# Optimization experiments

Hardware: AMD Instinct MI355X
Metric: run time of the kernel (lower is better)

## Reference

```python
import jax, jax.numpy as jnp
import numpy as np

C = 256
C8 = C // 8
B, H, W = 4, 64, 64


def setup_inputs() -> dict:
    key = jax.random.key(0)
    ks = jax.random.split(key, 10)
    s = lambda fan_in: 1.0 / np.sqrt(fan_in)
    return {
        "x": jax.random.normal(ks[0], (B, C, H, W), dtype=jnp.float32),
        "conv_w": jax.random.normal(ks[1], (C8, C), dtype=jnp.float32) * s(C),
        "conv_b": jax.random.normal(ks[2], (C8,), dtype=jnp.float32) * 0.01,
        "q_w": jax.random.normal(ks[3], (C8, C8), dtype=jnp.float32) * s(C8),
        "q_b": jax.random.normal(ks[4], (C8,), dtype=jnp.float32) * 0.01,
        "k_w": jax.random.normal(ks[5], (C8, C8), dtype=jnp.float32) * s(C8),
        "k_b": jax.random.normal(ks[6], (C8,), dtype=jnp.float32) * 0.01,
        "v_w": jax.random.normal(ks[7], (C, C8), dtype=jnp.float32) * s(C8),
        "v_b": jax.random.normal(ks[8], (C,), dtype=jnp.float32) * 0.01,
        "gamma": jax.random.normal(ks[9], (1,), dtype=jnp.float32) * 0.1,
    }


def reference(x, conv_w, conv_b, q_w, q_b, k_w, k_b, v_w, v_b, gamma):
    b, c, h, w = x.shape
    hw = h * w
    # 1x1 convs are channel-mixing matmuls over flattened spatial dims
    xf = x.reshape(b, c, hw)                                   # [B, C, HW]
    proj = jnp.einsum('dc,bcn->bdn', conv_w, xf) + conv_b[None, :, None]   # [B, C8, HW]
    q = jnp.einsum('ed,bdn->bne', q_w, proj) + q_b[None, None, :]          # [B, HW, C8]
    k = jnp.einsum('ed,bdn->ben', k_w, proj) + k_b[None, :, None]          # [B, C8, HW]
    v = jnp.einsum('cd,bdn->bcn', v_w, proj) + v_b[None, :, None]          # [B, C, HW]
    attn = jax.nn.softmax(jnp.einsum('bne,bem->bnm', q, k), axis=-1)       # [B, HW, HW]
    out = jnp.einsum('bcm,bnm->bcn', v, attn)                              # [B, C, HW]
    out = out.reshape(b, c, h, w)
    return gamma[0] * out + x
```

## Files before the change

kernel.cpp:

```cpp
#include <hip/hip_runtime.h>
#include <hip/hip_bf16.h>
#include <stdint.h>

#define B_   4
#define C_   256
#define C8_  32
#define HW_  4096
#define ROWS_ 320
#define MS_  4
#define L2E  1.4426950408889634f

typedef __attribute__((ext_vector_type(8)))  short  short8;
typedef __attribute__((ext_vector_type(8)))  ushort us8;
typedef __attribute__((ext_vector_type(16))) float  f32x16;

#define WT_OFF    0
#define BALL_OFF  (256*320*4)
#define Q_OFF     (BALL_OFF + 1280)
#define KT_OFF    (Q_OFF  + B_*HW_*C8_*2)
#define V_OFF     (KT_OFF + B_*HW_*C8_*2)
#define PACC_OFF  (V_OFF  + B_*C_*HW_*2)
#define LPART_OFF (PACC_OFF + (size_t)MS_*B_*C_*HW_*2)

__device__ __forceinline__ ushort f2bf(float f) {
    union { float f; uint32_t u; } v; v.f = f;
    uint32_t u = v.u;
    uint32_t r = u + 0x7fffu + ((u >> 16) & 1u);
    return (ushort)(r >> 16);
}
__device__ __forceinline__ uint32_t pktr(float lo, float hi) {
    union { float f; uint32_t u; } a, b; a.f = lo; b.f = hi;
    return __builtin_amdgcn_perm(b.u, a.u, 0x07060302u);
}
__device__ __forceinline__ float fexp2(float s) {
    float y = fmaf(s, 8388608.0f, 1064992506.0f);
    y = fmaxf(y, 0.0f);
    union { int i; float f; } c; c.i = (int)y;
    return c.f;
}

__global__ __launch_bounds__(256) void k_setup(
    const float* __restrict__ conv_w, const float* __restrict__ conv_b,
    const float* __restrict__ q_w, const float* __restrict__ q_b,
    const float* __restrict__ k_w, const float* __restrict__ k_b,
    const float* __restrict__ v_w, const float* __restrict__ v_b,
    ushort* __restrict__ wbf, float* __restrict__ ball)
{
    int r = blockIdx.x;
    int c = threadIdx.x;
    const float* wrow;
    float bias;
    if (r < 32)       { wrow = q_w + r*32;      bias = q_b[r];      }
    else if (r < 64)  { wrow = k_w + (r-32)*32; bias = k_b[r-32];   }
    else              { wrow = v_w + (r-64)*32; bias = v_b[r-64];   }
    float acc = 0.f;
    #pragma unroll
    for (int d = 0; d < 32; ++d) acc += wrow[d] * conv_w[d*C_ + c];
    float scale = (r < 32) ? L2E : 1.0f;
    int lanew = (r & 31) + 32*((c >> 3) & 1);
    int fidx  = (c >> 4)*10 + (r >> 5);
    wbf[fidx*512 + lanew*8 + (c & 7)] = f2bf(acc * scale);
    if (c == 0) {
        float bb = bias;
        #pragma unroll
        for (int d = 0; d < 32; ++d) bb += wrow[d] * conv_b[d];
        ball[r] = bb * scale;
    }
}

__global__ __launch_bounds__(320) void k_qkv(
    const float* __restrict__ x, const ushort* __restrict__ wbf,
    const float* __restrict__ ball,
    ushort* __restrict__ qg, ushort* __restrict__ ktg, ushort* __restrict__ vg)
{
    __shared__ ushort tr[5][32*40];

    int blk = blockIdx.x;
    int b  = blk >> 7;
    int nt = blk & 127;
    int n0 = nt * 32;
    int t = threadIdx.x;
    int w = t >> 6, lane = t & 63;
    int l31 = lane & 31, h = lane >> 5;

    f32x16 acc[2];
    acc[0] = (f32x16)(0.f);
    acc[1] = (f32x16)(0.f);

    const float* xb = x + (size_t)b*C_*HW_ + n0 + l31;

    #pragma unroll 2
    for (int kc = 0; kc < 16; ++kc) {
        short8 a0 = *(const short8*)(wbf + (kc*10 + w*2    )*512 + lane*8);
        short8 a1 = *(const short8*)(wbf + (kc*10 + w*2 + 1)*512 + lane*8);
        const float* xc = xb + (size_t)(kc*16 + h*8)*HW_;
        union { uint32_t d[4]; short8 s8; } bf;
        #pragma unroll
        for (int j2 = 0; j2 < 4; ++j2) {
            float f0 = xc[(size_t)(2*j2    )*HW_];
            float f1 = xc[(size_t)(2*j2 + 1)*HW_];
            bf.d[j2] = pktr(f0, f1);
        }
        acc[0] = __builtin_amdgcn_mfma_f32_32x32x16_bf16(a0, bf.s8, acc[0], 0, 0, 0);
        acc[1] = __builtin_amdgcn_mfma_f32_32x32x16_bf16(a1, bf.s8, acc[1], 0, 0, 0);
    }

    #pragma unroll
    for (int mi = 0; mi < 2; ++mi) {
        int rowb = w*64 + mi*32;
        bool isQK = (rowb < 64);
        #pragma unroll
        for (int r = 0; r < 16; ++r) {
            int roff = (r & 3) + 8*(r >> 2) + 4*h;
            ushort bv = f2bf(acc[mi][r] + ball[rowb + roff]);
            int ad = isQK ? (l31*40 + roff) : (roff*40 + l31);
            tr[w][ad] = bv;
        }
        __syncthreads();
        #pragma unroll
        for (int f = 0; f < 2; ++f) {
            us8 frag = *(const us8*)(&tr[w][l31*40 + f*16 + h*8]);
            if (isQK) {
                ushort* dstb = (rowb == 0) ? qg : ktg;
                size_t ad = ((size_t)((b*128 + nt)*2 + f) << 9) + lane*8;
                *(us8*)(dstb + ad) = frag;
            } else {
                int cblk = (rowb - 64) >> 5;
                int mb = nt*2 + f;
                size_t ad = ((size_t)((b*8 + cblk)*256 + mb) << 9) + lane*8;
                *(us8*)(vg + ad) = frag;
            }
        }
        __syncthreads();
    }
}

__global__ __launch_bounds__(512, 4) void k_attn(
    const ushort* __restrict__ qg, const ushort* __restrict__ ktg,
    const ushort* __restrict__ vg,
    ushort* __restrict__ pacc, float* __restrict__ lpart)
{
    __shared__ ushort v_lds[2][16*512];
    __shared__ ushort kt_lds[2][4*512];

    int blk = blockIdx.x;
    int ms = blk & 3;
    int cs = (blk >> 2) & 1;
    int qb = (blk >> 3) & 15;
    int b  = blk >> 7;
    int t = threadIdx.x;
    int w = t >> 6, lane = t & 63;
    int l31 = lane & 31, h = lane >> 5;
    int mbase = ms*1024;

    short8 qf[2];
    #pragma unroll
    for (int ks = 0; ks < 2; ++ks)
        qf[ks] = *(const short8*)(qg
            + ((size_t)((b*128 + qb*8 + w)*2 + ks) << 9) + lane*8);

    f32x16 acc[4];
    #pragma unroll
    for (int j = 0; j < 4; ++j) acc[j] = (f32x16)(0.f);
    float lsum = 0.f;

    #define STAGE(buf, m0)                                                          \
    {                                                                               \
        _Pragma("unroll")                                                           \
        for (int ff = 0; ff < 2; ++ff) {                                            \
            int f = w*2 + ff;                                                       \
            int cfr = f >> 2, mf = f & 3;                                           \
            const ushort* src = vg + ((size_t)((b*8 + cs*4 + cfr)*256               \
                                 + ((m0) >> 4) + mf) << 9) + lane*8;                \
            __builtin_amdgcn_global_load_lds(                                       \
                (const __attribute__((address_space(1))) uint32_t*)src,             \
                (__attribute__((address_space(3))) uint32_t*)&v_lds[buf][f*512],    \
                16, 0, 0);                                                          \
        }                                                                           \
        if (w < 4) {                                                                \
            const ushort* src = ktg + ((size_t)((b*128 + ((m0) >> 5) + (w >> 1))*2  \
                                 + (w & 1)) << 9) + lane*8;                         \
            __builtin_amdgcn_global_load_lds(                                       \
                (const __attribute__((address_space(1))) uint32_t*)src,             \
                (__attribute__((address_space(3))) uint32_t*)&kt_lds[buf][w*512],   \
                16, 0, 0);                                                          \
        }                                                                           \
    }

    STAGE(0, mbase)
    __syncthreads();

    int buf = 0;
    for (int it = 0; it < 16; ++it) {
        if (it + 1 < 16) STAGE(buf ^ 1, mbase + (it+1)*64)

        #pragma unroll
        for (int kb = 0; kb < 2; ++kb) {
            short8 kt0 = *(const short8*)(&kt_lds[buf][(kb*2+0)*512 + lane*8]);
            short8 kt1 = *(const short8*)(&kt_lds[buf][(kb*2+1)*512 + lane*8]);

            f32x16 s = (f32x16)(0.f);
            s = __builtin_amdgcn_mfma_f32_32x32x16_bf16(kt0, qf[0], s, 0, 0, 0);
            s = __builtin_amdgcn_mfma_f32_32x32x16_bf16(kt1, qf[1], s, 0, 0, 0);
            float e[16];
            #pragma unroll
            for (int r = 0; r < 16; ++r) e[r] = fexp2(s[r]);
            float t0 = 0.f, t1 = 0.f;
            #pragma unroll
            for (int r = 0; r < 8; ++r) { t0 += e[2*r]; t1 += e[2*r+1]; }
            lsum += t0 + t1;
            uint32_t u[8];
            #pragma unroll
            for (int i = 0; i < 8; ++i) u[i] = pktr(e[2*i], e[2*i+1]);

            uint32_t bpA = (uint32_t)__shfl_xor((int)(h ? u[0] : u[2]), 32);
            uint32_t bpB = (uint32_t)__shfl_xor((int)(h ? u[1] : u[3]), 32);
            uint32_t bpC = (uint32_t)__shfl_xor((int)(h ? u[4] : u[6]), 32);
            uint32_t bpD = (uint32_t)__shfl_xor((int)(h ? u[5] : u[7]), 32);
            union { uint32_t d[4]; short8 s8; } fe, fo;
            fe.d[0] = h ? bpA : u[0];  fe.d[1] = h ? bpB : u[1];
            fe.d[2] = h ? u[2] : bpA;  fe.d[3] = h ? u[3] : bpB;
            fo.d[0] = h ? bpC : u[4];  fo.d[1] = h ? bpD : u[5];
            fo.d[2] = h ? u[6] : bpC;  fo.d[3] = h ? u[7] : bpD;
            short8 pf0 = fe.s8;
            short8 pf1 = fo.s8;

            #pragma unroll
            for (int msub = 0; msub < 2; ++msub) {
                int ks16 = kb*2 + msub;
                short8 pfm = msub ? pf1 : pf0;
                #pragma unroll
                for (int cfr = 0; cfr < 4; ++cfr) {
                    short8 vf = *(const short8*)(&v_lds[buf][(cfr*4 + ks16)*512 + lane*8]);
                    acc[cfr] = __builtin_amdgcn_mfma_f32_32x32x16_bf16(vf, pfm, acc[cfr], 0, 0, 0);
                }
            }
        }
        __syncthreads();
        buf ^= 1;
    }

    {
        union { float f; int i; } cv; cv.f = lsum;
        cv.i = __shfl_xor(cv.i, 32);
        lsum += cv.f;
    }
    if (cs == 0 && h == 0)
        lpart[(size_t)(ms*B_ + b)*HW_ + qb*256 + w*32 + l31] = lsum;

    int blkl = ((ms*B_ + b)*16 + qb)*2 + cs;
    #pragma unroll
    for (int cfr = 0; cfr < 4; ++cfr) {
        union { uint32_t d[8]; us8 hlf[2]; } pk;
        #pragma unroll
        for (int i = 0; i < 8; ++i)
            pk.d[i] = pktr(acc[cfr][2*i], acc[cfr][2*i+1]);
        ushort* dst = pacc + ((size_t)(blkl*32 + w*4 + cfr) << 10);
        *(us8*)(dst + lane*8)       = pk.hlf[0];
        *(us8*)(dst + 512 + lane*8) = pk.hlf[1];
    }
    #undef STAGE
}

__global__ __launch_bounds__(256) void k_comb(
    const ushort* __restrict__ pacc, const float* __restrict__ lpart,
    const float* __restrict__ x, const float* __restrict__ gamma_p,
    float* __restrict__ out)
{
    int gid = blockIdx.x * 256 + threadIdx.x;
    int l31 = gid & 31;
    int h   = (gid >> 5) & 1;
    int cfr = (gid >> 6) & 3;
    int w   = (gid >> 8) & 7;
    int cs  = (gid >> 11) & 1;
    int qb  = (gid >> 12) & 15;
    int b   = (gid >> 16) & 3;

    int q = qb*256 + w*32 + l31;
    int frag = w*4 + cfr;
    int lane = h*32 + l31;

    float sum[16];
    #pragma unroll
    for (int k = 0; k < 16; ++k) sum[k] = 0.f;
    float lt = 0.f;

    #pragma unroll
    for (int ms = 0; ms < MS_; ++ms) {
        int blkl = ((ms*B_ + b)*16 + qb)*2 + cs;
        const ushort* pp = pacc + ((size_t)(blkl*32 + frag) << 10) + lane*8;
        us8 a0 = *(const us8*)pp;
        us8 a1 = *(const us8*)(pp + 512);
        #pragma unroll
        for (int k = 0; k < 8; ++k) {
            union { uint32_t u; float f; } cv;
            cv.u = ((uint32_t)a0[k]) << 16;  sum[k]   += cv.f;
            cv.u = ((uint32_t)a1[k]) << 16;  sum[k+8] += cv.f;
        }
        lt += lpart[(size_t)(ms*B_ + b)*HW_ + q];
    }

    float g = gamma_p[0];
    float rl = g / lt;
    const float* xb = x + (size_t)b*C_*HW_ + q;
    float* ob = out + (size_t)b*C_*HW_ + q;
    #pragma unroll
    for (int k = 0; k < 16; ++k) {
        int c = cs*128 + cfr*32 + (k & 3) + 8*(k >> 2) + 4*h;
        size_t idx = (size_t)c*HW_;
        ob[idx] = sum[k]*rl + xb[idx];
    }
}

extern "C" void kernel_launch(void* const* d_in, const int* in_sizes, int n_in,
                              void* d_out, int out_size, void* d_ws, size_t ws_size,
                              hipStream_t stream)
{
    const float* x      = (const float*)d_in[0];
    const float* conv_w = (const float*)d_in[1];
    const float* conv_b = (const float*)d_in[2];
    const float* q_w    = (const float*)d_in[3];
    const float* q_b    = (const float*)d_in[4];
    const float* k_w    = (const float*)d_in[5];
    const float* k_b    = (const float*)d_in[6];
    const float* v_w    = (const float*)d_in[7];
    const float* v_b    = (const float*)d_in[8];
    const float* gamma  = (const float*)d_in[9];
    float* out = (float*)d_out;

    char* ws = (char*)d_ws;
    ushort* wbf   = (ushort*)(ws + WT_OFF);
    float*  ball  = (float*)(ws + BALL_OFF);
    ushort* qg    = (ushort*)(ws + Q_OFF);
    ushort* ktg   = (ushort*)(ws + KT_OFF);
    ushort* vg    = (ushort*)(ws + V_OFF);
    ushort* pacc  = (ushort*)(ws + PACC_OFF);
    float*  lpart = (float*)(ws + LPART_OFF);

    k_setup<<<ROWS_, 256, 0, stream>>>(conv_w, conv_b, q_w, q_b, k_w, k_b,
                                       v_w, v_b, wbf, ball);
    k_qkv<<<B_*128, 320, 0, stream>>>(x, wbf, ball, qg, ktg, vg);
    k_attn<<<512, 512, 0, stream>>>(qg, ktg, vg, pacc, lpart);
    k_comb<<<(B_*C_*HW_/16)/256, 256, 0, stream>>>(pacc, lpart, x, gamma, out);
}
```

Measured before the change: 162.4 us.

## Double attention K-tile per stage and stage combine output through LDS for float4 stores

The attention kernel now stages 128 keys per pipeline step instead of 64, halving the loop iterations and barriers but doubling LDS use per block, which may lower occupancy. The combine kernel is restructured so each block handles one 32-query by 128-channel tile. Scaled partial sums are written to a padded LDS buffer and then read back as float4, so the residual loads of x and the output stores become wide and coalesced rather than scattered 4-byte accesses.

```diff
diff --git a/kernel.cpp b/kernel.cpp
--- a/kernel.cpp
+++ b/kernel.cpp
@@ -140,8 +140,8 @@
     const ushort* __restrict__ vg,
     ushort* __restrict__ pacc, float* __restrict__ lpart)
 {
-    __shared__ ushort v_lds[2][16*512];
-    __shared__ ushort kt_lds[2][4*512];
+    __shared__ ushort v_lds[2][32*512];
+    __shared__ ushort kt_lds[2][8*512];
 
     int blk = blockIdx.x;
     int ms = blk & 3;
@@ -167,9 +167,9 @@
     #define STAGE(buf, m0)                                                          \
     {                                                                               \
         _Pragma("unroll")                                                           \
-        for (int ff = 0; ff < 2; ++ff) {                                            \
-            int f = w*2 + ff;                                                       \
-            int cfr = f >> 2, mf = f & 3;                                           \
+        for (int ff = 0; ff < 4; ++ff) {                                            \
+            int f = w*4 + ff;                                                       \
+            int cfr = f >> 3, mf = f & 7;                                           \
             const ushort* src = vg + ((size_t)((b*8 + cs*4 + cfr)*256               \
                                  + ((m0) >> 4) + mf) << 9) + lane*8;                \
             __builtin_amdgcn_global_load_lds(                                       \
@@ -177,7 +177,7 @@
                 (__attribute__((address_space(3))) uint32_t*)&v_lds[buf][f*512],    \
                 16, 0, 0);                                                          \
         }                                                                           \
-        if (w < 4) {                                                                \
+        {                                                                           \
             const ushort* src = ktg + ((size_t)((b*128 + ((m0) >> 5) + (w >> 1))*2  \
                                  + (w & 1)) << 9) + lane*8;                         \
             __builtin_amdgcn_global_load_lds(                                       \
@@ -191,11 +191,11 @@
     __syncthreads();
 
     int buf = 0;
-    for (int it = 0; it < 16; ++it) {
-        if (it + 1 < 16) STAGE(buf ^ 1, mbase + (it+1)*64)
-
-        #pragma unroll
-        for (int kb = 0; kb < 2; ++kb) {
+    for (int it = 0; it < 8; ++it) {
+        if (it + 1 < 8) STAGE(buf ^ 1, mbase + (it+1)*128)
+
+        #pragma unroll
+        for (int kb = 0; kb < 4; ++kb) {
             short8 kt0 = *(const short8*)(&kt_lds[buf][(kb*2+0)*512 + lane*8]);
             short8 kt1 = *(const short8*)(&kt_lds[buf][(kb*2+1)*512 + lane*8]);
 
@@ -231,7 +231,7 @@
                 short8 pfm = msub ? pf1 : pf0;
                 #pragma unroll
                 for (int cfr = 0; cfr < 4; ++cfr) {
-                    short8 vf = *(const short8*)(&v_lds[buf][(cfr*4 + ks16)*512 + lane*8]);
+                    short8 vf = *(const short8*)(&v_lds[buf][(cfr*8 + ks16)*512 + lane*8]);
                     acc[cfr] = __builtin_amdgcn_mfma_f32_32x32x16_bf16(vf, pfm, acc[cfr], 0, 0, 0);
                 }
             }
@@ -267,18 +267,20 @@
     const float* __restrict__ x, const float* __restrict__ gamma_p,
     float* __restrict__ out)
 {
-    int gid = blockIdx.x * 256 + threadIdx.x;
-    int l31 = gid & 31;
-    int h   = (gid >> 5) & 1;
-    int cfr = (gid >> 6) & 3;
-    int w   = (gid >> 8) & 7;
-    int cs  = (gid >> 11) & 1;
-    int qb  = (gid >> 12) & 15;
-    int b   = (gid >> 16) & 3;
-
+    __shared__ float lds_acc[128*36];
+
+    int blk = blockIdx.x;
+    int w  = blk & 7;
+    int cs = (blk >> 3) & 1;
+    int qb = (blk >> 4) & 15;
+    int b  = blk >> 8;
+    int t = threadIdx.x;
+
+    int l31 = t & 31;
+    int h   = (t >> 5) & 1;
+    int cfr = (t >> 6) & 3;
     int q = qb*256 + w*32 + l31;
-    int frag = w*4 + cfr;
-    int lane = h*32 + l31;
+    int lanef = h*32 + l31;
 
     float sum[16];
     #pragma unroll
@@ -288,7 +290,7 @@
     #pragma unroll
     for (int ms = 0; ms < MS_; ++ms) {
         int blkl = ((ms*B_ + b)*16 + qb)*2 + cs;
-        const ushort* pp = pacc + ((size_t)(blkl*32 + frag) << 10) + lane*8;
+        const ushort* pp = pacc + ((size_t)(blkl*32 + w*4 + cfr) << 10) + lanef*8;
         us8 a0 = *(const us8*)pp;
         us8 a1 = *(const us8*)(pp + 512);
         #pragma unroll
@@ -300,15 +302,25 @@
         lt += lpart[(size_t)(ms*B_ + b)*HW_ + q];
     }
 
-    float g = gamma_p[0];
-    float rl = g / lt;
-    const float* xb = x + (size_t)b*C_*HW_ + q;
-    float* ob = out + (size_t)b*C_*HW_ + q;
+    float rl = gamma_p[0] / lt;
     #pragma unroll
     for (int k = 0; k < 16; ++k) {
-        int c = cs*128 + cfr*32 + (k & 3) + 8*(k >> 2) + 4*h;
-        size_t idx = (size_t)c*HW_;
-        ob[idx] = sum[k]*rl + xb[idx];
+        int c = cfr*32 + (k & 3) + 8*(k >> 2) + 4*h;
+        lds_acc[c*36 + l31] = sum[k]*rl;
+    }
+    __syncthreads();
+
+    const float* xb = x + ((size_t)(b*C_ + cs*128))*HW_ + qb*256 + w*32;
+    float* ob = out + ((size_t)(b*C_ + cs*128))*HW_ + qb*256 + w*32;
+    #pragma unroll
+    for (int i = 0; i < 4; ++i) {
+        int s = t + i*256;
+        int c = s >> 3, qg = s & 7;
+        float4 a = *(const float4*)(&lds_acc[c*36 + qg*4]);
+        size_t off = (size_t)c*HW_ + qg*4;
+        float4 xv = *(const float4*)(xb + off);
+        a.x += xv.x; a.y += xv.y; a.z += xv.z; a.w += xv.w;
+        *(float4*)(ob + off) = a;
     }
 }
 
@@ -341,5 +353,5 @@
                                        v_w, v_b, wbf, ball);
     k_qkv<<<B_*128, 320, 0, stream>>>(x, wbf, ball, qg, ktg, vg);
     k_attn<<<512, 512, 0, stream>>>(qg, ktg, vg, pacc, lpart);
-    k_comb<<<(B_*C_*HW_/16)/256, 256, 0, stream>>>(pacc, lpart, x, gamma, out);
-}
+    k_comb<<<1024, 256, 0, stream>>>(pacc, lpart, x, gamma, out);
+}
```

Measured after the change: 252.9 us. 55.8% more time.
